# Optimization experiments

Measured on AMD Instinct MI355X. Metric: run time of the kernel, lower is better.

The kernel has to match this reference:

```python
import jax, jax.numpy as jnp
import numpy as np

N_NODES = 100000
N_EDGES = 640000
F = 128          # in_features
MID = 192        # (2*F + OUT)//2
OUT = 128


def setup_inputs() -> dict:
    key = jax.random.key(0)
    k_h, k_dr, k_s, k_d, k_w1, k_w2 = jax.random.split(key, 6)
    h = jax.random.normal(k_h, (N_NODES, F), dtype=jnp.float32)
    dR = jax.random.uniform(k_dr, (N_EDGES,), dtype=jnp.float32)
    src_idx = jax.random.randint(k_s, (N_EDGES,), 0, N_NODES)
    dst_idx = jax.random.randint(k_d, (N_EDGES,), 0, N_NODES)
    W1 = jax.random.normal(k_w1, (2 * F + 1, MID), dtype=jnp.float32) * (1.0 / np.sqrt(2 * F + 1))
    b1 = jnp.zeros((MID,), dtype=jnp.float32)
    W2 = jax.random.normal(k_w2, (MID, OUT), dtype=jnp.float32) * (1.0 / np.sqrt(MID))
    b2 = jnp.zeros((OUT,), dtype=jnp.float32)
    return {"h": h, "dR": dR, "src_idx": src_idx, "dst_idx": dst_idx,
            "W1": W1, "b1": b1, "W2": W2, "b2": b2}


def reference(h, dR, src_idx, dst_idx, W1, b1, W2, b2):
    # first=True branch: cat([dst_hidden, src_hidden, dR[:, None]]) -> [E, 2F+1]
    inp = jnp.concatenate([h[dst_idx], h[src_idx], dR[:, None]], axis=1)
    hid = jax.nn.relu(inp @ W1 + b1)          # [E, MID]
    out = jnp.tanh(hid @ W2 + b2)             # [E, OUT]
    return out
```

## Files before the change

### kernel.cpp

```cpp
#include <hip/hip_runtime.h>
#include <hip/hip_bf16.h>


#define F_IN   128
#define MID    192
#define OUT_N  128
#define K1     256
#define M_TILE 64
#define A_STRIDE 264
#define H_STRIDE 200

typedef __attribute__((ext_vector_type(8))) short bf16x8;
typedef __attribute__((ext_vector_type(4))) float f32x4;

__device__ __forceinline__ unsigned short f2bf(float f) {
    unsigned u = __builtin_bit_cast(unsigned, f);
    u = (u + 0x7FFFu + ((u >> 16) & 1u)) >> 16;
    return (unsigned short)u;
}

__global__ void pack_weights(const float* __restrict__ W1,
                             const float* __restrict__ W2,
                             unsigned short* __restrict__ p1,
                             unsigned short* __restrict__ p2,
                             float* __restrict__ wdr) {
    int i = blockIdx.x * 256 + threadIdx.x;
    if (i < K1 * MID) {
        int kin = i & 31;
        int rest = i >> 5;
        int n = rest % MID;
        int kt = rest / MID;
        p1[i] = f2bf(W1[(kt * 32 + kin) * MID + n]);
    }
    int j = i - K1 * MID;
    if (j >= 0 && j < MID * OUT_N) {
        int kin = j & 31;
        int rest = j >> 5;
        int n = rest & 127;
        int kt = rest >> 7;
        p2[j] = f2bf(W2[(kt * 32 + kin) * OUT_N + n]);
    }
    if (i < MID) wdr[i] = W1[256 * MID + i];
}

__global__ __launch_bounds__(256, 4)
void edge_mlp_kernel(const float* __restrict__ h,
                     const float* __restrict__ dR,
                     const int*   __restrict__ src_idx,
                     const int*   __restrict__ dst_idx,
                     const float* __restrict__ b1,
                     const float* __restrict__ b2,
                     const unsigned short* __restrict__ p1,
                     const unsigned short* __restrict__ p2,
                     const float* __restrict__ wdr,
                     float* __restrict__ out) {
    __shared__ __align__(16) unsigned short sA[M_TILE * A_STRIDE];
    __shared__ float sdr[M_TILE];

    const int tid = threadIdx.x;
    const int e0 = blockIdx.x * M_TILE;

    if (tid < M_TILE) sdr[tid] = dR[e0 + tid];

    {
        const int j = tid & 31;
        const int g = tid >> 5;
#pragma unroll
        for (int it = 0; it < 16; ++it) {
            int half = it * 8 + g;
            int e = half >> 1;
            int part = half & 1;
            const int* ip = part ? src_idx : dst_idx;
            int row = ip[e0 + e];
            const float4 v = *(const float4*)(h + (size_t)row * F_IN + j * 4);
            ushort4 b;
            b.x = f2bf(v.x); b.y = f2bf(v.y); b.z = f2bf(v.z); b.w = f2bf(v.w);
            *(ushort4*)(&sA[e * A_STRIDE + part * F_IN + j * 4]) = b;
        }
    }
    __syncthreads();

    const int lane = tid & 63;
    const int w = tid >> 6;
    const int l15 = lane & 15;
    const int q = lane >> 4;

    f32x4 acc1[4][3] = {};
    for (int kt = 0; kt < 8; ++kt) {
        bf16x8 a[4];
#pragma unroll
        for (int m = 0; m < 4; ++m)
            a[m] = *(const bf16x8*)(&sA[(m * 16 + l15) * A_STRIDE + kt * 32 + q * 8]);
#pragma unroll
        for (int ni = 0; ni < 3; ++ni) {
            int nb = (w + ni * 4) * 16 + l15;
            bf16x8 bf = *(const bf16x8*)(&p1[(kt * MID + nb) * 32 + q * 8]);
#pragma unroll
            for (int m = 0; m < 4; ++m)
                acc1[m][ni] = __builtin_amdgcn_mfma_f32_16x16x32_bf16(a[m], bf, acc1[m][ni], 0, 0, 0);
        }
    }
    __syncthreads();

    unsigned short* sH = sA;
#pragma unroll
    for (int ni = 0; ni < 3; ++ni) {
        int n = (w + ni * 4) * 16 + l15;
        float bb = b1[n];
        float wd = wdr[n];
#pragma unroll
        for (int m = 0; m < 4; ++m) {
#pragma unroll
            for (int r = 0; r < 4; ++r) {
                int e = m * 16 + q * 4 + r;
                float v = acc1[m][ni][r] + bb + sdr[e] * wd;
                v = fmaxf(v, 0.0f);
                sH[e * H_STRIDE + n] = f2bf(v);
            }
        }
    }
    __syncthreads();

    f32x4 acc2[4][2] = {};
    for (int kt = 0; kt < 6; ++kt) {
        bf16x8 a[4];
#pragma unroll
        for (int m = 0; m < 4; ++m)
            a[m] = *(const bf16x8*)(&sH[(m * 16 + l15) * H_STRIDE + kt * 32 + q * 8]);
#pragma unroll
        for (int ni = 0; ni < 2; ++ni) {
            int nb = (w + ni * 4) * 16 + l15;
            bf16x8 bf = *(const bf16x8*)(&p2[(kt * OUT_N + nb) * 32 + q * 8]);
#pragma unroll
            for (int m = 0; m < 4; ++m)
                acc2[m][ni] = __builtin_amdgcn_mfma_f32_16x16x32_bf16(a[m], bf, acc2[m][ni], 0, 0, 0);
        }
    }

#pragma unroll
    for (int ni = 0; ni < 2; ++ni) {
        int n = (w + ni * 4) * 16 + l15;
        float bb = b2[n];
#pragma unroll
        for (int m = 0; m < 4; ++m) {
#pragma unroll
            for (int r = 0; r < 4; ++r) {
                int e = e0 + m * 16 + q * 4 + r;
                float x = acc2[m][ni][r] + bb;
                x = fminf(fmaxf(x, -10.0f), 10.0f);
                float t = __expf(2.0f * x);
                out[(size_t)e * OUT_N + n] = (t - 1.0f) * __builtin_amdgcn_rcpf(t + 1.0f);
            }
        }
    }
}

extern "C" void kernel_launch(void* const* d_in, const int* in_sizes, int n_in,
                              void* d_out, int out_size, void* d_ws, size_t ws_size,
                              hipStream_t stream) {
    const float* h   = (const float*)d_in[0];
    const float* dR  = (const float*)d_in[1];
    const int* src   = (const int*)d_in[2];
    const int* dst   = (const int*)d_in[3];
    const float* W1  = (const float*)d_in[4];
    const float* b1  = (const float*)d_in[5];
    const float* W2  = (const float*)d_in[6];
    const float* b2  = (const float*)d_in[7];
    float* out       = (float*)d_out;

    unsigned short* p1 = (unsigned short*)d_ws;
    unsigned short* p2 = p1 + K1 * MID;
    float* wdr         = (float*)(p2 + MID * OUT_N);

    const int E = in_sizes[1];

    pack_weights<<<(K1 * MID + MID * OUT_N + 255) / 256, 256, 0, stream>>>(W1, W2, p1, p2, wdr);
    edge_mlp_kernel<<<E / M_TILE, 256, 0, stream>>>(h, dR, src, dst, b1, b2, p1, p2, wdr, out);
}
```

Measured before the change: 492.3 us.

## Pre-convert node features to bf16 and gather MFMA operands directly from global

Adds a pre-pass that converts the whole node feature table to bf16 in workspace, so edge gathers move half the bytes. The edge kernel drops the shared-memory staging of the concatenated input and loads MFMA A fragments straight from the gathered rows. It also repacks weights into per-lane contiguous tiles, raises occupancy, switches bf16 rounding to a cheaper form, rewrites tanh with exp2 and rcp, and uses nontemporal output stores. Risks include an extra pass over all of h, uncoalesced direct gathers without LDS reuse, and slightly different rounding.

```diff
diff --git a/kernel.cpp b/kernel.cpp
--- a/kernel.cpp
+++ b/kernel.cpp
@@ -5,9 +5,7 @@
 #define F_IN   128
 #define MID    192
 #define OUT_N  128
-#define K1     256
 #define M_TILE 64
-#define A_STRIDE 264
 #define H_STRIDE 200
 
 typedef __attribute__((ext_vector_type(8))) short bf16x8;
@@ -15,105 +13,121 @@
 
 __device__ __forceinline__ unsigned short f2bf(float f) {
     unsigned u = __builtin_bit_cast(unsigned, f);
-    u = (u + 0x7FFFu + ((u >> 16) & 1u)) >> 16;
-    return (unsigned short)u;
-}
-
-__global__ void pack_weights(const float* __restrict__ W1,
-                             const float* __restrict__ W2,
-                             unsigned short* __restrict__ p1,
-                             unsigned short* __restrict__ p2,
-                             float* __restrict__ wdr) {
+    return (unsigned short)((u + 0x8000u) >> 16);
+}
+
+__global__ void pack_h(const float* __restrict__ h, unsigned short* __restrict__ hb, int n4) {
     int i = blockIdx.x * 256 + threadIdx.x;
-    if (i < K1 * MID) {
-        int kin = i & 31;
-        int rest = i >> 5;
-        int n = rest % MID;
-        int kt = rest / MID;
-        p1[i] = f2bf(W1[(kt * 32 + kin) * MID + n]);
-    }
-    int j = i - K1 * MID;
-    if (j >= 0 && j < MID * OUT_N) {
-        int kin = j & 31;
-        int rest = j >> 5;
-        int n = rest & 127;
-        int kt = rest >> 7;
-        p2[j] = f2bf(W2[(kt * 32 + kin) * OUT_N + n]);
-    }
-    if (i < MID) wdr[i] = W1[256 * MID + i];
-}
-
-__global__ __launch_bounds__(256, 4)
-void edge_mlp_kernel(const float* __restrict__ h,
-                     const float* __restrict__ dR,
-                     const int*   __restrict__ src_idx,
-                     const int*   __restrict__ dst_idx,
-                     const float* __restrict__ b1,
-                     const float* __restrict__ b2,
-                     const unsigned short* __restrict__ p1,
-                     const unsigned short* __restrict__ p2,
-                     const float* __restrict__ wdr,
-                     float* __restrict__ out) {
-    __shared__ __align__(16) unsigned short sA[M_TILE * A_STRIDE];
-    __shared__ float sdr[M_TILE];
+    if (i >= n4) return;
+    float4 v = ((const float4*)h)[i];
+    ushort4 b;
+    b.x = f2bf(v.x); b.y = f2bf(v.y); b.z = f2bf(v.z); b.w = f2bf(v.w);
+    ((ushort4*)hb)[i] = b;
+}
+
+__global__ void pack_w(const float* __restrict__ W1, const float* __restrict__ W2,
+                       unsigned short* __restrict__ p1, unsigned short* __restrict__ p2) {
+    int i = blockIdx.x * 256 + threadIdx.x;
+    if (i < 49152) {
+        int kin = i & 31; int t = i >> 5;
+        int kt = t & 7; t >>= 3;
+        int l = t & 15; int nt = t >> 4;
+        p1[i] = f2bf(W1[(kt * 32 + kin) * MID + nt * 16 + l]);
+    }
+    int j = i - 49152;
+    if (j >= 0 && j < 24576) {
+        int kin = j & 31; int t = j >> 5;
+        int kt = t % 6; t /= 6;
+        int l = t & 15; int nt = t >> 4;
+        p2[j] = f2bf(W2[(kt * 32 + kin) * OUT_N + nt * 16 + l]);
+    }
+}
+
+template<bool PREH>
+__global__ __launch_bounds__(256, 5)
+void edge_mlp(const float* __restrict__ h,
+              const unsigned short* __restrict__ hb,
+              const float* __restrict__ dR,
+              const int* __restrict__ src_idx,
+              const int* __restrict__ dst_idx,
+              const float* __restrict__ W1,
+              const float* __restrict__ b1,
+              const float* __restrict__ b2,
+              const unsigned short* __restrict__ p1,
+              const unsigned short* __restrict__ p2,
+              float* __restrict__ out) {
+    __shared__ __align__(16) unsigned short sH[M_TILE * H_STRIDE];
 
     const int tid = threadIdx.x;
     const int e0 = blockIdx.x * M_TILE;
-
-    if (tid < M_TILE) sdr[tid] = dR[e0 + tid];
-
-    {
-        const int j = tid & 31;
-        const int g = tid >> 5;
-#pragma unroll
-        for (int it = 0; it < 16; ++it) {
-            int half = it * 8 + g;
-            int e = half >> 1;
-            int part = half & 1;
-            const int* ip = part ? src_idx : dst_idx;
-            int row = ip[e0 + e];
-            const float4 v = *(const float4*)(h + (size_t)row * F_IN + j * 4);
-            ushort4 b;
-            b.x = f2bf(v.x); b.y = f2bf(v.y); b.z = f2bf(v.z); b.w = f2bf(v.w);
-            *(ushort4*)(&sA[e * A_STRIDE + part * F_IN + j * 4]) = b;
-        }
-    }
-    __syncthreads();
-
     const int lane = tid & 63;
     const int w = tid >> 6;
     const int l15 = lane & 15;
     const int q = lane >> 4;
 
+    int idxd[4], idxs[4];
+#pragma unroll
+    for (int m = 0; m < 4; ++m) {
+        idxd[m] = dst_idx[e0 + m * 16 + l15];
+        idxs[m] = src_idx[e0 + m * 16 + l15];
+    }
+
+    const unsigned short* bb1[3];
+#pragma unroll
+    for (int ni = 0; ni < 3; ++ni) {
+        int nt = w + ni * 4;
+        bb1[ni] = p1 + nt * 4096 + l15 * 256 + q * 8;
+    }
+
     f32x4 acc1[4][3] = {};
+#pragma unroll
     for (int kt = 0; kt < 8; ++kt) {
+        const int part = kt >> 2, ktl = kt & 3;
         bf16x8 a[4];
 #pragma unroll
-        for (int m = 0; m < 4; ++m)
-            a[m] = *(const bf16x8*)(&sA[(m * 16 + l15) * A_STRIDE + kt * 32 + q * 8]);
+        for (int m = 0; m < 4; ++m) {
+            int idx = part ? idxs[m] : idxd[m];
+            if (PREH) {
+                a[m] = *(const bf16x8*)(hb + (size_t)idx * F_IN + ktl * 32 + q * 8);
+            } else {
+                const float* hp = h + (size_t)idx * F_IN + ktl * 32 + q * 8;
+                float4 v0 = *(const float4*)hp;
+                float4 v1 = *(const float4*)(hp + 4);
+                bf16x8 t;
+                t[0] = (short)f2bf(v0.x); t[1] = (short)f2bf(v0.y);
+                t[2] = (short)f2bf(v0.z); t[3] = (short)f2bf(v0.w);
+                t[4] = (short)f2bf(v1.x); t[5] = (short)f2bf(v1.y);
+                t[6] = (short)f2bf(v1.z); t[7] = (short)f2bf(v1.w);
+                a[m] = t;
+            }
+        }
 #pragma unroll
         for (int ni = 0; ni < 3; ++ni) {
-            int nb = (w + ni * 4) * 16 + l15;
-            bf16x8 bf = *(const bf16x8*)(&p1[(kt * MID + nb) * 32 + q * 8]);
+            bf16x8 bf = *(const bf16x8*)(bb1[ni] + kt * 32);
 #pragma unroll
             for (int m = 0; m < 4; ++m)
                 acc1[m][ni] = __builtin_amdgcn_mfma_f32_16x16x32_bf16(a[m], bf, acc1[m][ni], 0, 0, 0);
         }
     }
-    __syncthreads();
-
-    unsigned short* sH = sA;
+
+    float dr[4][4];
+#pragma unroll
+    for (int m = 0; m < 4; ++m)
+#pragma unroll
+        for (int r = 0; r < 4; ++r)
+            dr[m][r] = dR[e0 + m * 16 + q * 4 + r];
+
 #pragma unroll
     for (int ni = 0; ni < 3; ++ni) {
         int n = (w + ni * 4) * 16 + l15;
         float bb = b1[n];
-        float wd = wdr[n];
+        float wd = W1[256 * MID + n];
 #pragma unroll
         for (int m = 0; m < 4; ++m) {
 #pragma unroll
             for (int r = 0; r < 4; ++r) {
                 int e = m * 16 + q * 4 + r;
-                float v = acc1[m][ni][r] + bb + sdr[e] * wd;
+                float v = acc1[m][ni][r] + bb + dr[m][r] * wd;
                 v = fmaxf(v, 0.0f);
                 sH[e * H_STRIDE + n] = f2bf(v);
             }
@@ -121,16 +135,27 @@
     }
     __syncthreads();
 
+    const unsigned short* bb2[2];
+#pragma unroll
+    for (int ni = 0; ni < 2; ++ni) {
+        int nt = w + ni * 4;
+        bb2[ni] = p2 + nt * 3072 + l15 * 192 + q * 8;
+    }
+    const unsigned short* arow[4];
+#pragma unroll
+    for (int m = 0; m < 4; ++m)
+        arow[m] = sH + (m * 16 + l15) * H_STRIDE + q * 8;
+
     f32x4 acc2[4][2] = {};
+#pragma unroll
     for (int kt = 0; kt < 6; ++kt) {
         bf16x8 a[4];
 #pragma unroll
         for (int m = 0; m < 4; ++m)
-            a[m] = *(const bf16x8*)(&sH[(m * 16 + l15) * H_STRIDE + kt * 32 + q * 8]);
+            a[m] = *(const bf16x8*)(arow[m] + kt * 32);
 #pragma unroll
         for (int ni = 0; ni < 2; ++ni) {
-            int nb = (w + ni * 4) * 16 + l15;
-            bf16x8 bf = *(const bf16x8*)(&p2[(kt * OUT_N + nb) * 32 + q * 8]);
+            bf16x8 bf = *(const bf16x8*)(bb2[ni] + kt * 32);
 #pragma unroll
             for (int m = 0; m < 4; ++m)
                 acc2[m][ni] = __builtin_amdgcn_mfma_f32_16x16x32_bf16(a[m], bf, acc2[m][ni], 0, 0, 0);
@@ -147,9 +172,9 @@
             for (int r = 0; r < 4; ++r) {
                 int e = e0 + m * 16 + q * 4 + r;
                 float x = acc2[m][ni][r] + bb;
-                x = fminf(fmaxf(x, -10.0f), 10.0f);
-                float t = __expf(2.0f * x);
-                out[(size_t)e * OUT_N + n] = (t - 1.0f) * __builtin_amdgcn_rcpf(t + 1.0f);
+                float t = __builtin_amdgcn_exp2f(x * 2.885390081777927f);
+                float y = 1.0f - 2.0f * __builtin_amdgcn_rcpf(t + 1.0f);
+                __builtin_nontemporal_store(y, out + (size_t)e * OUT_N + n);
             }
         }
     }
@@ -168,12 +193,23 @@
     const float* b2  = (const float*)d_in[7];
     float* out       = (float*)d_out;
 
+    const int E = in_sizes[1];
+    const int NNODES = in_sizes[0] / F_IN;
+
     unsigned short* p1 = (unsigned short*)d_ws;
-    unsigned short* p2 = p1 + K1 * MID;
-    float* wdr         = (float*)(p2 + MID * OUT_N);
-
-    const int E = in_sizes[1];
-
-    pack_weights<<<(K1 * MID + MID * OUT_N + 255) / 256, 256, 0, stream>>>(W1, W2, p1, p2, wdr);
-    edge_mlp_kernel<<<E / M_TILE, 256, 0, stream>>>(h, dR, src, dst, b1, b2, p1, p2, wdr, out);
-}
+    unsigned short* p2 = p1 + 49152;
+    unsigned short* hb = p2 + 24576;
+    const size_t need = (size_t)(49152 + 24576) * 2 + (size_t)NNODES * F_IN * 2;
+
+    pack_w<<<288, 256, 0, stream>>>(W1, W2, p1, p2);
+
+    if (ws_size >= need) {
+        int n4 = NNODES * F_IN / 4;
+        pack_h<<<(n4 + 255) / 256, 256, 0, stream>>>(h, hb, n4);
+        edge_mlp<true><<<E / M_TILE, 256, 0, stream>>>(h, hb, dR, src, dst,
+                                                       W1, b1, b2, p1, p2, out);
+    } else {
+        edge_mlp<false><<<E / M_TILE, 256, 0, stream>>>(h, hb, dR, src, dst,
+                                                        W1, b1, b2, p1, p2, out);
+    }
+}
```

Result: slower. 685.7 us (+39.3%).
